# Kernel optimization log

Measured on AMD Instinct MI355X. Metric: run time of the kernel, lower is better.

## Reference

```python
import jax, jax.numpy as jnp
import numpy as np

B, T, E, H = 2, 4096, 1024, 16
SEGS = (256, 512, 1024, 2048, 4096)
DILS = (1, 2, 4, 8, 16)
NEG = -1e8  # torchscale uses -1e8 for uncovered / masked lse entries


def setup_inputs() -> dict:
    key = jax.random.key(0)
    ks = jax.random.split(key, 5)
    sc = 0.02
    zb = jnp.zeros((E,), jnp.float32)
    return {
        "x": jax.random.normal(ks[0], (B, T, E), jnp.float32),
        "wq": jax.random.normal(ks[1], (E, E), jnp.float32) * sc,
        "bq": zb,
        "wk": jax.random.normal(ks[2], (E, E), jnp.float32) * sc,
        "bk": zb,
        "wv": jax.random.normal(ks[3], (E, E), jnp.float32) * sc,
        "bv": zb,
        "wo": jax.random.normal(ks[4], (E, E), jnp.float32) * sc,
        "bo": zb,
    }


def _scale_attn(q, k, v, w, r):
    # One LongNet scale: segment length w, dilation ratio r.
    # Head group g = head // (H//r) attends to in-segment positions p with p % r == g
    # (torchscale dense_to_sparse diagonal over (r1, r2)).
    Bq, Tq, Hq, d = q.shape
    n, s, hp = Tq // w, w // r, Hq // r  # segments, sparse length, heads per group

    def gather(x):
        # [B,T,H,d] -> segments [B,n,w,H,d]; split w=(s,r1) (p=l*r+r1) and H=(r2,hp);
        # keep diagonal r1 == r2.
        x = x.reshape(Bq, n, s, r, r, hp, d)
        x = jnp.diagonal(x, axis1=3, axis2=4)          # [B,n,s,hp,d,r]
        return jnp.moveaxis(x, -1, 3).reshape(Bq, n, s, Hq, d)

    qs, ks_, vs = gather(q), gather(k), gather(v)
    scores = jnp.einsum('bnqhd,bnkhd->bnhqk', qs, ks_)
    mask = jnp.tril(jnp.ones((s, s), dtype=bool))       # causal within sparse segment
    scores = jnp.where(mask, scores, NEG)
    lse = jax.scipy.special.logsumexp(scores, axis=-1)  # [B,n,h,q]
    out = jnp.einsum('bnhqk,bnkhd->bnqhd', jax.nn.softmax(scores, axis=-1), vs)

    # Scatter back to dense positions (sparse_to_dense): uncovered -> out 0, lse -1e8.
    eye = jnp.eye(r, dtype=out.dtype)
    out_g = out.reshape(Bq, n, s, r, hp, d)                               # heads as (g, hp)
    dense = jnp.einsum('bnsghd,pg->bnspghd', out_g, eye).reshape(Bq, Tq, Hq, d)
    lse_g = jnp.transpose(lse, (0, 1, 3, 2)).reshape(Bq, n, s, r, hp)     # [B,n,s,g,hp]
    lse_d = jnp.where(eye[:, :, None] > 0, lse_g[:, :, :, None, :, :], NEG)
    return dense, lse_d.reshape(Bq, Tq, Hq)


def reference(x, wq, bq, wk, bk, wv, bv, wo, bo):
    d = E // H
    q = (x @ wq + bq).reshape(B, T, H, d) * (d ** -0.5)
    k = (x @ wk + bk).reshape(B, T, H, d)
    v = (x @ wv + bv).reshape(B, T, H, d)
    outs, lses = [], []
    for w_, r_ in zip(SEGS, DILS):
        o, l = _scale_attn(q, k, v, w_, r_)
        outs.append(o)
        lses.append(l)
    # Merge scales with softmax over per-scale log-sum-exp (dense-attention equivalence).
    wgt = jax.nn.softmax(jnp.stack(lses), axis=0)[..., None]  # [S,B,T,H,1]
    y = jnp.sum(jnp.stack(outs) * wgt, axis=0).reshape(B, T, E)
    return y @ wo + bo
```

## Files before the change

### kernel.cpp

```cpp
#include <hip/hip_runtime.h>
#include <hip/hip_bf16.h>

typedef __bf16 bf16_t;
typedef __bf16 bf16x8 __attribute__((ext_vector_type(8)));
typedef __bf16 bf16x4 __attribute__((ext_vector_type(4)));
typedef float f32x4 __attribute__((ext_vector_type(4)));
typedef int vint4 __attribute__((ext_vector_type(4)));

#define AS1 __attribute__((address_space(1)))
#define AS3 __attribute__((address_space(3)))

constexpr int B_ = 2, T_ = 4096, E_ = 1024, H_ = 16;
constexpr int M_ = B_ * T_;

__device__ constexpr size_t OB_OFF[5]  = {0, 8388608, 12582912, 14680064, 15728640};
__device__ constexpr size_t LSE_OFF[5] = {0, 131072, 196608, 229376, 245760};
constexpr size_t OB_TOTAL  = 16252928;
constexpr size_t LSE_TOTAL = 253952;

__global__ __launch_bounds__(256) void cvt_f32_bf16(const float* __restrict__ in,
                                                    bf16_t* __restrict__ out) {
  int i = (blockIdx.x * 256 + threadIdx.x) * 4;
  const float4 v = *(const float4*)(in + i);
  bf16x4 o;
  o[0] = (bf16_t)v.x; o[1] = (bf16_t)v.y; o[2] = (bf16_t)v.z; o[3] = (bf16_t)v.w;
  *(bf16x4*)(out + i) = o;
}

__global__ __launch_bounds__(256) void cvt_transpose_w(
    const float* __restrict__ w0, const float* __restrict__ w1,
    const float* __restrict__ w2, const float* __restrict__ w3,
    bf16_t* __restrict__ o0, bf16_t* __restrict__ o1,
    bf16_t* __restrict__ o2, bf16_t* __restrict__ o3) {
  __shared__ float tile[32][33];
  const float* src; bf16_t* dst;
  switch (blockIdx.z) {
    case 0: src = w0; dst = o0; break;
    case 1: src = w1; dst = o1; break;
    case 2: src = w2; dst = o2; break;
    default: src = w3; dst = o3; break;
  }
  const int n0 = blockIdx.x * 32, k0 = blockIdx.y * 32;
  const int tx = threadIdx.x & 31, ty = threadIdx.x >> 5;
#pragma unroll
  for (int i = 0; i < 32; i += 8)
    tile[ty + i][tx] = src[(size_t)(k0 + ty + i) * E_ + n0 + tx];
  __syncthreads();
#pragma unroll
  for (int i = 0; i < 32; i += 8)
    dst[(size_t)(n0 + ty + i) * E_ + k0 + tx] = (bf16_t)tile[tx][ty + i];
}

template <bool OUT_BF16, bool QKV>
__global__ __launch_bounds__(512, 1) void gemm8p(
    const bf16_t* __restrict__ A, const bf16_t* __restrict__ BT,
    const float* __restrict__ bias0, const float* __restrict__ bias1,
    const float* __restrict__ bias2, void* __restrict__ Cout) {
  constexpr int K = E_;
  constexpr int NKT = K / 64;
  __shared__ bf16_t Sm[73728];

  const int tid = threadIdx.x;
  const int lane = tid & 63;
  const int wid = tid >> 6;
  const int wm = wid >> 2, wn = wid & 3;
  const int lc = lane & 15, lg = lane >> 4;
  const int bm = blockIdx.x;
  int bn = blockIdx.y;

  const float* bias = bias0;
  float scale = 1.0f;
  void* outp = Cout;
  const bf16_t* Bt = BT;
  if (QKV) {
    const int which = bn >> 2;
    bn &= 3;
    bias = (which == 0) ? bias0 : (which == 1) ? bias1 : bias2;
    scale = (which == 0) ? 0.125f : 1.0f;
    outp = (void*)((bf16_t*)Cout + (size_t)which * M_ * E_);
    Bt += (size_t)which * E_ * E_;
  }

  const int srow = tid >> 3;
  const int schunk = (tid & 7) ^ (srow & 7);
  const bf16_t* Ag = A + (size_t)(bm * 128 + srow) * K + schunk * 8;
  const bf16_t* Bg = Bt + (size_t)(bn * 256 + srow) * K + schunk * 8;

  const int sl0 = (lg ^ (lc & 7)) * 8;
  const int sl1 = ((4 + lg) ^ (lc & 7)) * 8;

  f32x4 acc[4][4] = {};

  auto stA = [&](int kt, int bu, int l) {
    __builtin_amdgcn_global_load_lds(
        (const AS1 void*)(Ag + (size_t)(l * 64) * K + kt * 64),
        (AS3 void*)(Sm + bu * 8192 + l * 4096 + tid * 8), 16, 0, 0);
  };
  auto stB = [&](int kt, int bu, int l) {
    __builtin_amdgcn_global_load_lds(
        (const AS1 void*)(Bg + (size_t)(l * 64) * K + kt * 64),
        (AS3 void*)(Sm + 24576 + bu * 16384 + l * 4096 + tid * 8), 16, 0, 0);
  };

  stA(0, 0, 0); stA(0, 0, 1);
  stB(0, 0, 0); stB(0, 0, 1); stB(0, 0, 2); stB(0, 0, 3);
  stA(1, 1, 0); stA(1, 1, 1);
  stB(1, 1, 0); stB(1, 1, 1); stB(1, 1, 2); stB(1, 1, 3);
  asm volatile("s_waitcnt vmcnt(6)" ::: "memory");
  __builtin_amdgcn_s_barrier();

  for (int kt = 0; kt < NKT; ++kt) {
    const int bc = kt % 3;
    const int bs = (kt + 2) % 3;
    const bool st = (kt + 2) < NKT;
    const int arow = bc * 8192 + (wm * 64 + lc) * 64;
    const int brow = 24576 + bc * 16384 + (wn * 64 + lc) * 64;

#pragma unroll
    for (int ph = 0; ph < 2; ++ph) {
      bf16x8 afr[2][2], bfr[4][2];
#pragma unroll
      for (int i2 = 0; i2 < 2; ++i2) {
        const int rb = arow + (ph * 32 + i2 * 16) * 64;
        afr[i2][0] = *(const bf16x8*)&Sm[rb + sl0];
        afr[i2][1] = *(const bf16x8*)&Sm[rb + sl1];
      }
#pragma unroll
      for (int j = 0; j < 4; ++j) {
        const int rb = brow + j * 16 * 64;
        bfr[j][0] = *(const bf16x8*)&Sm[rb + sl0];
        bfr[j][1] = *(const bf16x8*)&Sm[rb + sl1];
      }
      if (st) {
        if (ph == 0) { stA(kt + 2, bs, 0); stB(kt + 2, bs, 0); stB(kt + 2, bs, 1); }
        else         { stA(kt + 2, bs, 1); stB(kt + 2, bs, 2); stB(kt + 2, bs, 3); }
      }
      __builtin_amdgcn_s_barrier();
      asm volatile("s_waitcnt lgkmcnt(0)" ::: "memory");
      __builtin_amdgcn_s_setprio(1);
#pragma unroll
      for (int i2 = 0; i2 < 2; ++i2)
#pragma unroll
        for (int j = 0; j < 4; ++j) {
          acc[ph * 2 + i2][j] = __builtin_amdgcn_mfma_f32_16x16x32_bf16(
              afr[i2][0], bfr[j][0], acc[ph * 2 + i2][j], 0, 0, 0);
          acc[ph * 2 + i2][j] = __builtin_amdgcn_mfma_f32_16x16x32_bf16(
              afr[i2][1], bfr[j][1], acc[ph * 2 + i2][j], 0, 0, 0);
        }
      __builtin_amdgcn_s_setprio(0);
      if (ph == 1) {
        if (st) asm volatile("s_waitcnt vmcnt(6)" ::: "memory");
        else    asm volatile("s_waitcnt vmcnt(0)" ::: "memory");
      }
      __builtin_amdgcn_s_barrier();
    }
  }

#pragma unroll
  for (int i = 0; i < 4; ++i) {
    const int row = bm * 128 + wm * 64 + i * 16 + lg * 4;
#pragma unroll
    for (int j = 0; j < 4; ++j) {
      const int col = bn * 256 + wn * 64 + j * 16 + lc;
      const float bv = bias[col];
#pragma unroll
      for (int rg = 0; rg < 4; ++rg) {
        const float v = (acc[i][j][rg] + bv) * scale;
        if (OUT_BF16)
          ((bf16_t*)outp)[(size_t)(row + rg) * E_ + col] = (bf16_t)v;
        else
          ((float*)outp)[(size_t)(row + rg) * E_ + col] = v;
      }
    }
  }
}

__global__ __launch_bounds__(512, 4) void attn_inst(
    const bf16_t* __restrict__ Q, const bf16_t* __restrict__ K,
    const bf16_t* __restrict__ V, bf16_t* __restrict__ Ob,
    float* __restrict__ Lse) {
  __shared__ alignas(16) bf16_t Ks[256][72];
  __shared__ alignas(16) bf16_t Vt[64][264];
  __shared__ alignas(16) bf16_t Pw[8][16][40];

  const int bid = blockIdx.x;
  int s, ibase;
  if (bid < 512)      { s = 0; ibase = 0; }
  else if (bid < 768) { s = 1; ibase = 512; }
  else if (bid < 896) { s = 2; ibase = 768; }
  else if (bid < 960) { s = 3; ibase = 896; }
  else                { s = 4; ibase = 960; }
  const int inst = bid - ibase;
  const int h = inst & 15;
  const int nseg_log = 4 - s;
  const int seg = (inst >> 4) & ((1 << nseg_log) - 1);
  const int b = inst >> (4 + nseg_log);
  const int g = h >> (4 - s);

  const int t = threadIdx.x;
  const int lane = t & 63;
  const int wv = t >> 6;
  const int lc = lane & 15;
  const int lg = lane >> 4;

  {
    const int row = t >> 1, ch = (t & 1) * 32;
    const int tk = ((seg * 256 + row) << s) + g;
    const size_t off = ((size_t)b * T_ + tk) * E_ + h * 64 + ch;
    const bf16_t* Kg = K + off;
    const bf16_t* Vg = V + off;
#pragma unroll
    for (int j = 0; j < 4; ++j)
      *(bf16x8*)&Ks[row][ch + j * 8] = *(const bf16x8*)(Kg + j * 8);
#pragma unroll
    for (int j = 0; j < 4; ++j) {
      bf16x8 va = *(const bf16x8*)(Vg + j * 8);
#pragma unroll
      for (int e = 0; e < 8; ++e) Vt[ch + j * 8 + e][row] = va[e];
    }
  }
  __syncthreads();

  const size_t rowbase = (size_t)(b * H_ + h) * (T_ >> s) + seg * 256;

#pragma unroll
  for (int sel = 0; sel < 2; ++sel) {
    const int tile = sel ? (15 - wv) : wv;
    const int q = tile * 16 + lc;

    const int tq = ((seg * 256 + q) << s) + g;
    const bf16_t* Qg = Q + ((size_t)b * T_ + tq) * E_ + h * 64 + lg * 8;
    bf16x8 qfrag0 = *(const bf16x8*)(Qg);
    bf16x8 qfrag1 = *(const bf16x8*)(Qg + 32);

    float m = -INFINITY, Z = 0.0f;
    f32x4 Oa[4] = {};

    const int nkb = tile / 2 + 1;
    const int diag = tile / 2;
    for (int kb = 0; kb < nkb; ++kb) {
      f32x4 sacc[2] = {};
      __builtin_amdgcn_s_setprio(1);
#pragma unroll
      for (int kt = 0; kt < 2; ++kt) {
        bf16x8 kf0 = *(const bf16x8*)&Ks[kb * 32 + kt * 16 + lc][lg * 8];
        bf16x8 kf1 = *(const bf16x8*)&Ks[kb * 32 + kt * 16 + lc][32 + lg * 8];
        sacc[kt] = __builtin_amdgcn_mfma_f32_16x16x32_bf16(kf0, qfrag0, sacc[kt], 0, 0, 0);
        sacc[kt] = __builtin_amdgcn_mfma_f32_16x16x32_bf16(kf1, qfrag1, sacc[kt], 0, 0, 0);
      }
      __builtin_amdgcn_s_setprio(0);
      if (kb == diag) {
#pragma unroll
        for (int kt = 0; kt < 2; ++kt)
#pragma unroll
          for (int rg = 0; rg < 4; ++rg)
            if (kb * 32 + kt * 16 + lg * 4 + rg > q) sacc[kt][rg] = -1e30f;
      }
      float pm = fmaxf(fmaxf(fmaxf(sacc[0][0], sacc[0][1]), fmaxf(sacc[0][2], sacc[0][3])),
                       fmaxf(fmaxf(sacc[1][0], sacc[1][1]), fmaxf(sacc[1][2], sacc[1][3])));
      pm = fmaxf(pm, __shfl_xor(pm, 16));
      pm = fmaxf(pm, __shfl_xor(pm, 32));
      const float nm = fmaxf(m, pm);
      const float crr = __expf(m - nm);
      m = nm;
      float psum = 0.0f;
#pragma unroll
      for (int kt = 0; kt < 2; ++kt)
#pragma unroll
        for (int rg = 0; rg < 4; ++rg) {
          const float p = __expf(sacc[kt][rg] - nm);
          psum += p;
          Pw[wv][lc][kt * 16 + lg * 4 + rg] = (bf16_t)p;
        }
      psum += __shfl_xor(psum, 16);
      psum += __shfl_xor(psum, 32);
      Z = Z * crr + psum;
#pragma unroll
      for (int dt = 0; dt < 4; ++dt)
#pragma unroll
        for (int rg = 0; rg < 4; ++rg) Oa[dt][rg] *= crr;
      bf16x8 pb = *(const bf16x8*)&Pw[wv][lc][lg * 8];
      __builtin_amdgcn_s_setprio(1);
#pragma unroll
      for (int dt = 0; dt < 4; ++dt) {
        bf16x8 vf = *(const bf16x8*)&Vt[dt * 16 + lc][kb * 32 + lg * 8];
        Oa[dt] = __builtin_amdgcn_mfma_f32_16x16x32_bf16(vf, pb, Oa[dt], 0, 0, 0);
      }
      __builtin_amdgcn_s_setprio(0);
    }

    const float lse = m + __logf(Z);
    const float iZ = 1.0f / Z;
    bf16_t* orow = Ob + OB_OFF[s] + (rowbase + q) * 64 + lg * 4;
#pragma unroll
    for (int dt = 0; dt < 4; ++dt) {
      bf16x4 ov;
      ov[0] = (bf16_t)(Oa[dt][0] * iZ);
      ov[1] = (bf16_t)(Oa[dt][1] * iZ);
      ov[2] = (bf16_t)(Oa[dt][2] * iZ);
      ov[3] = (bf16_t)(Oa[dt][3] * iZ);
      *(bf16x4*)(orow + dt * 16) = ov;
    }
    if (lg == 0) Lse[LSE_OFF[s] + rowbase + q] = lse;
  }
}

__global__ __launch_bounds__(256) void attn_merge(const bf16_t* __restrict__ Ob,
                                                  const float* __restrict__ Lse,
                                                  bf16_t* __restrict__ Y) {
  const int gtid = blockIdx.x * 256 + threadIdx.x;
  const int d8 = gtid & 7;
  const int h = (gtid >> 3) & 15;
  const int tt = (gtid >> 7) & (T_ - 1);
  const int b = gtid >> 19;

  float m = -INFINITY, S = 0.0f;
  float acc[8];
#pragma unroll
  for (int j = 0; j < 8; ++j) acc[j] = 0.0f;

#pragma unroll
  for (int s = 0; s < 5; ++s) {
    const int r = 1 << s;
    const int g = h >> (4 - s);
    if ((tt & (r - 1)) != g) continue;
    const size_t idx = (size_t)(b * H_ + h) * (T_ >> s) + (tt >> s);
    const float lse = Lse[LSE_OFF[s] + idx];
    const bf16x8 ov = *(const bf16x8*)(Ob + OB_OFF[s] + idx * 64 + d8 * 8);
    const float nM = fmaxf(m, lse);
    const float a = __expf(m - nM);
    const float e = __expf(lse - nM);
#pragma unroll
    for (int j = 0; j < 8; ++j) acc[j] = acc[j] * a + (float)ov[j] * e;
    S = S * a + e;
    m = nM;
  }

  const float invS = 1.0f / S;
  bf16x8 o;
#pragma unroll
  for (int j = 0; j < 8; ++j) o[j] = (bf16_t)(acc[j] * invS);
  *(bf16x8*)(Y + (size_t)gtid * 8) = o;
}

extern "C" void kernel_launch(void* const* d_in, const int* in_sizes, int n_in,
                              void* d_out, int out_size, void* d_ws, size_t ws_size,
                              hipStream_t stream) {
  (void)in_sizes; (void)n_in; (void)out_size; (void)ws_size;
  const float* x  = (const float*)d_in[0];
  const float* wq = (const float*)d_in[1];
  const float* bq = (const float*)d_in[2];
  const float* wk = (const float*)d_in[3];
  const float* bk = (const float*)d_in[4];
  const float* wv = (const float*)d_in[5];
  const float* bv = (const float*)d_in[6];
  const float* wo = (const float*)d_in[7];
  const float* bo = (const float*)d_in[8];

  char* p = (char*)d_ws;
  auto take = [&](size_t bytes) {
    char* q = p;
    p += (bytes + 255) & ~(size_t)255;
    return (void*)q;
  };
  bf16_t* wq_t = (bf16_t*)take((size_t)E_ * E_ * 2);
  bf16_t* wk_t = (bf16_t*)take((size_t)E_ * E_ * 2);
  bf16_t* wv_t = (bf16_t*)take((size_t)E_ * E_ * 2);
  bf16_t* wo_t = (bf16_t*)take((size_t)E_ * E_ * 2);
  bf16_t* xb   = (bf16_t*)take((size_t)M_ * E_ * 2);
  bf16_t* qb   = (bf16_t*)take((size_t)M_ * E_ * 2);
  bf16_t* kbuf = (bf16_t*)take((size_t)M_ * E_ * 2);
  bf16_t* vbuf = (bf16_t*)take((size_t)M_ * E_ * 2);
  bf16_t* yb   = (bf16_t*)take((size_t)M_ * E_ * 2);
  bf16_t* Ob   = (bf16_t*)take(OB_TOTAL * 2);
  float*  Lse  = (float*)take(LSE_TOTAL * 4);
  (void)wk_t; (void)wv_t;

  cvt_f32_bf16<<<M_ * E_ / 1024, 256, 0, stream>>>(x, xb);
  cvt_transpose_w<<<dim3(32, 32, 4), 256, 0, stream>>>(wq, wk, wv, wo, wq_t, wk_t, wv_t, wo_t);

  gemm8p<true, true><<<dim3(M_ / 128, 12), 512, 0, stream>>>(
      xb, wq_t, bq, bk, bv, qb);

  attn_inst<<<992, 512, 0, stream>>>(qb, kbuf, vbuf, Ob, Lse);

  attn_merge<<<M_ * E_ / 8 / 256, 256, 0, stream>>>(Ob, Lse, yb);

  gemm8p<false, false><<<dim3(M_ / 128, 4), 512, 0, stream>>>(
      yb, wo_t, bo, bo, bo, d_out);
}
```

Baseline: 147.4 us.

## Switch GEMM tiles to 256x128 with simpler single-phase triple-buffered pipeline

```diff
diff --git a/kernel.cpp b/kernel.cpp
--- a/kernel.cpp
+++ b/kernel.cpp
@@ -52,18 +52,18 @@
 }
 
 template <bool OUT_BF16, bool QKV>
-__global__ __launch_bounds__(512, 1) void gemm8p(
+__global__ __launch_bounds__(512, 1) void gemm_dp(
     const bf16_t* __restrict__ A, const bf16_t* __restrict__ BT,
     const float* __restrict__ bias0, const float* __restrict__ bias1,
     const float* __restrict__ bias2, void* __restrict__ Cout) {
   constexpr int K = E_;
-  constexpr int NKT = K / 64;
+  constexpr int NT = K / 64;
   __shared__ bf16_t Sm[73728];
 
   const int tid = threadIdx.x;
   const int lane = tid & 63;
   const int wid = tid >> 6;
-  const int wm = wid >> 2, wn = wid & 3;
+  const int wm = wid >> 1, wn = wid & 1;
   const int lc = lane & 15, lg = lane >> 4;
   const int bm = blockIdx.x;
   int bn = blockIdx.y;
@@ -73,8 +73,8 @@
   void* outp = Cout;
   const bf16_t* Bt = BT;
   if (QKV) {
-    const int which = bn >> 2;
-    bn &= 3;
+    const int which = bn >> 3;
+    bn &= 7;
     bias = (which == 0) ? bias0 : (which == 1) ? bias1 : bias2;
     scale = (which == 0) ? 0.125f : 1.0f;
     outp = (void*)((bf16_t*)Cout + (size_t)which * M_ * E_);
@@ -83,85 +83,76 @@
 
   const int srow = tid >> 3;
   const int schunk = (tid & 7) ^ (srow & 7);
-  const bf16_t* Ag = A + (size_t)(bm * 128 + srow) * K + schunk * 8;
-  const bf16_t* Bg = Bt + (size_t)(bn * 256 + srow) * K + schunk * 8;
-
-  const int sl0 = (lg ^ (lc & 7)) * 8;
+  const bf16_t* Ag = A + (size_t)(bm * 256 + srow) * K + schunk * 8;
+  const bf16_t* Bg = Bt + (size_t)(bn * 128 + srow) * K + schunk * 8;
+
+  auto stA = [&](int kt, int bu) {
+#pragma unroll
+    for (int l = 0; l < 4; ++l)
+      __builtin_amdgcn_global_load_lds(
+          (const AS1 void*)(Ag + (size_t)(l * 64) * K + kt * 64),
+          (AS3 void*)(Sm + bu * 16384 + l * 4096 + tid * 8), 16, 0, 0);
+  };
+  auto stB = [&](int kt, int bu) {
+#pragma unroll
+    for (int l = 0; l < 2; ++l)
+      __builtin_amdgcn_global_load_lds(
+          (const AS1 void*)(Bg + (size_t)(l * 64) * K + kt * 64),
+          (AS3 void*)(Sm + 49152 + bu * 8192 + l * 4096 + tid * 8), 16, 0, 0);
+  };
+
+  const int sl0 = ((lg) ^ (lc & 7)) * 8;
   const int sl1 = ((4 + lg) ^ (lc & 7)) * 8;
 
   f32x4 acc[4][4] = {};
 
-  auto stA = [&](int kt, int bu, int l) {
-    __builtin_amdgcn_global_load_lds(
-        (const AS1 void*)(Ag + (size_t)(l * 64) * K + kt * 64),
-        (AS3 void*)(Sm + bu * 8192 + l * 4096 + tid * 8), 16, 0, 0);
-  };
-  auto stB = [&](int kt, int bu, int l) {
-    __builtin_amdgcn_global_load_lds(
-        (const AS1 void*)(Bg + (size_t)(l * 64) * K + kt * 64),
-        (AS3 void*)(Sm + 24576 + bu * 16384 + l * 4096 + tid * 8), 16, 0, 0);
-  };
-
-  stA(0, 0, 0); stA(0, 0, 1);
-  stB(0, 0, 0); stB(0, 0, 1); stB(0, 0, 2); stB(0, 0, 3);
-  stA(1, 1, 0); stA(1, 1, 1);
-  stB(1, 1, 0); stB(1, 1, 1); stB(1, 1, 2); stB(1, 1, 3);
-  asm volatile("s_waitcnt vmcnt(6)" ::: "memory");
-  __builtin_amdgcn_s_barrier();
-
-  for (int kt = 0; kt < NKT; ++kt) {
+  stA(0, 0); stB(0, 0);
+  stA(1, 1); stB(1, 1);
+
+  for (int kt = 0; kt < NT; ++kt) {
     const int bc = kt % 3;
-    const int bs = (kt + 2) % 3;
-    const bool st = (kt + 2) < NKT;
-    const int arow = bc * 8192 + (wm * 64 + lc) * 64;
-    const int brow = 24576 + bc * 16384 + (wn * 64 + lc) * 64;
-
-#pragma unroll
-    for (int ph = 0; ph < 2; ++ph) {
-      bf16x8 afr[2][2], bfr[4][2];
-#pragma unroll
-      for (int i2 = 0; i2 < 2; ++i2) {
-        const int rb = arow + (ph * 32 + i2 * 16) * 64;
-        afr[i2][0] = *(const bf16x8*)&Sm[rb + sl0];
-        afr[i2][1] = *(const bf16x8*)&Sm[rb + sl1];
-      }
+    if (kt + 2 < NT) {
+      const int bs = (kt + 2) % 3;
+      stA(kt + 2, bs); stB(kt + 2, bs);
+      asm volatile("s_waitcnt vmcnt(12)" ::: "memory");
+    } else if (kt + 1 < NT) {
+      asm volatile("s_waitcnt vmcnt(6)" ::: "memory");
+    } else {
+      asm volatile("s_waitcnt vmcnt(0)" ::: "memory");
+    }
+    __builtin_amdgcn_s_barrier();
+    asm volatile("" ::: "memory");
+
+    const int ab = bc * 16384 + (wm * 64 + lc) * 64;
+    const int bb = 49152 + bc * 8192 + (wn * 64 + lc) * 64;
+    bf16x8 afr[4][2], bfr[4][2];
+#pragma unroll
+    for (int i = 0; i < 4; ++i) {
+      afr[i][0] = *(const bf16x8*)&Sm[ab + i * 1024 + sl0];
+      afr[i][1] = *(const bf16x8*)&Sm[ab + i * 1024 + sl1];
+    }
+#pragma unroll
+    for (int j = 0; j < 4; ++j) {
+      bfr[j][0] = *(const bf16x8*)&Sm[bb + j * 1024 + sl0];
+      bfr[j][1] = *(const bf16x8*)&Sm[bb + j * 1024 + sl1];
+    }
+#pragma unroll
+    for (int i = 0; i < 4; ++i)
 #pragma unroll
       for (int j = 0; j < 4; ++j) {
-        const int rb = brow + j * 16 * 64;
-        bfr[j][0] = *(const bf16x8*)&Sm[rb + sl0];
-        bfr[j][1] = *(const bf16x8*)&Sm[rb + sl1];
-      }
-      if (st) {
-        if (ph == 0) { stA(kt + 2, bs, 0); stB(kt + 2, bs, 0); stB(kt + 2, bs, 1); }
-        else         { stA(kt + 2, bs, 1); stB(kt + 2, bs, 2); stB(kt + 2, bs, 3); }
-      }
-      __builtin_amdgcn_s_barrier();
-      asm volatile("s_waitcnt lgkmcnt(0)" ::: "memory");
-      __builtin_amdgcn_s_setprio(1);
-#pragma unroll
-      for (int i2 = 0; i2 < 2; ++i2)
-#pragma unroll
-        for (int j = 0; j < 4; ++j) {
-          acc[ph * 2 + i2][j] = __builtin_amdgcn_mfma_f32_16x16x32_bf16(
-              afr[i2][0], bfr[j][0], acc[ph * 2 + i2][j], 0, 0, 0);
-          acc[ph * 2 + i2][j] = __builtin_amdgcn_mfma_f32_16x16x32_bf16(
-              afr[i2][1], bfr[j][1], acc[ph * 2 + i2][j], 0, 0, 0);
-        }
-      __builtin_amdgcn_s_setprio(0);
-      if (ph == 1) {
-        if (st) asm volatile("s_waitcnt vmcnt(6)" ::: "memory");
-        else    asm volatile("s_waitcnt vmcnt(0)" ::: "memory");
-      }
-      __builtin_amdgcn_s_barrier();
-    }
+        acc[i][j] = __builtin_amdgcn_mfma_f32_16x16x32_bf16(afr[i][0], bfr[j][0], acc[i][j], 0, 0, 0);
+        acc[i][j] = __builtin_amdgcn_mfma_f32_16x16x32_bf16(afr[i][1], bfr[j][1], acc[i][j], 0, 0, 0);
+      }
+    asm volatile("" ::: "memory");
+    __builtin_amdgcn_s_barrier();
   }
 
 #pragma unroll
   for (int i = 0; i < 4; ++i) {
-    const int row = bm * 128 + wm * 64 + i * 16 + lg * 4;
+    const int row = bm * 256 + wm * 64 + i * 16 + lg * 4;
 #pragma unroll
     for (int j = 0; j < 4; ++j) {
-      const int col = bn * 256 + wn * 64 + j * 16 + lc;
+      const int col = bn * 128 + wn * 64 + j * 16 + lc;
       const float bv = bias[col];
 #pragma unroll
       for (int rg = 0; rg < 4; ++rg) {
@@ -379,13 +370,13 @@
   cvt_f32_bf16<<<M_ * E_ / 1024, 256, 0, stream>>>(x, xb);
   cvt_transpose_w<<<dim3(32, 32, 4), 256, 0, stream>>>(wq, wk, wv, wo, wq_t, wk_t, wv_t, wo_t);
 
-  gemm8p<true, true><<<dim3(M_ / 128, 12), 512, 0, stream>>>(
+  gemm_dp<true, true><<<dim3(M_ / 256, 24), 512, 0, stream>>>(
       xb, wq_t, bq, bk, bv, qb);
 
   attn_inst<<<992, 512, 0, stream>>>(qb, kbuf, vbuf, Ob, Lse);
 
   attn_merge<<<M_ * E_ / 8 / 256, 256, 0, stream>>>(Ob, Lse, yb);
 
-  gemm8p<false, false><<<dim3(M_ / 128, 4), 512, 0, stream>>>(
+  gemm_dp<false, false><<<dim3(M_ / 256, 8), 512, 0, stream>>>(
       yb, wo_t, bo, bo, bo, d_out);
 }
```

New measurement: 138.0 us. -6.4%, faster.
